# Optimization experiments

Hardware: AMD Instinct MI355X
Metric: run time of the kernel (lower is better)

Reference implementation:

```python
import jax, jax.numpy as jnp
import numpy as np

NUM_HEADS = 8
DIM_NODE, DIM_EDGE, DIM_TIME, DIM_OUT = 512, 172, 100, 512
U_NODE, U_EDGE, U_TIME, NUM_DST, E = 100000, 8192, 50000, 16384, 131072


def _linear_params(k, fan_in, fan_out):
    # torch.nn.Linear default init: U(-1/sqrt(fan_in), 1/sqrt(fan_in))
    kw, kb = jax.random.split(k)
    bound = 1.0 / np.sqrt(fan_in)
    w = jax.random.uniform(kw, (fan_in, fan_out), jnp.float32, -bound, bound)
    b = jax.random.uniform(kb, (fan_out,), jnp.float32, -bound, bound)
    return w, b


def setup_inputs() -> dict:
    key = jax.random.key(0)
    ks = jax.random.split(key, 16)
    inp = {}
    inp["idx"] = jax.random.randint(ks[0], (E,), 0, NUM_DST, jnp.int32)
    inp["nodeData"] = jax.random.normal(ks[1], (U_NODE, DIM_NODE), jnp.float32)
    inp["node_inverse"] = jax.random.randint(ks[2], (E,), 0, U_NODE, jnp.int32)
    inp["node_dst_inverse"] = jax.random.randint(ks[3], (NUM_DST,), 0, U_NODE, jnp.int32)
    inp["efeat_unique"] = jax.random.normal(ks[4], (U_EDGE, DIM_EDGE), jnp.float32)
    inp["efeat_inverse"] = jax.random.randint(ks[5], (E,), 0, U_EDGE, jnp.int32)
    inp["time_unique"] = jax.random.normal(ks[6], (U_TIME, DIM_TIME), jnp.float32)
    inp["time_inverse"] = jax.random.randint(ks[7], (E,), 0, U_TIME, jnp.int32)
    inp["time_dst_unique"] = jax.random.normal(ks[8], (1, DIM_TIME), jnp.float32)
    inp["time_dst_inverse"] = jnp.zeros((NUM_DST,), jnp.int32)
    inp["wq_node_w"], inp["wq_node_b"] = _linear_params(ks[9], DIM_NODE, DIM_OUT)
    inp["wq_time_w"], inp["wq_time_b"] = _linear_params(ks[10], DIM_TIME, DIM_OUT)
    inp["wkv_node_w"], inp["wkv_node_b"] = _linear_params(ks[11], DIM_NODE, 2 * DIM_OUT)
    inp["wkv_edge_w"], inp["wkv_edge_b"] = _linear_params(ks[12], DIM_EDGE, 2 * DIM_OUT)
    inp["wkv_time_w"], inp["wkv_time_b"] = _linear_params(ks[13], DIM_TIME, 2 * DIM_OUT)
    return inp


def reference(idx, nodeData, node_inverse, node_dst_inverse, efeat_unique,
              efeat_inverse, time_unique, time_inverse, time_dst_unique,
              time_dst_inverse, wq_node_w, wq_node_b, wq_time_w, wq_time_b,
              wkv_node_w, wkv_node_b, wkv_edge_w, wkv_edge_b, wkv_time_w,
              wkv_time_b):
    # project on UNIQUE rows, then scatter via inverse indices (dedup pattern)
    q_node = (nodeData @ wq_node_w + wq_node_b)[node_dst_inverse]      # [num_dst, D]
    q_time = (time_dst_unique @ wq_time_w + wq_time_b)[time_dst_inverse]
    Q = (q_node + q_time)[idx]                                          # [E, D]
    z_node = (nodeData @ wkv_node_w + wkv_node_b)[node_inverse]         # [E, 2D]
    z_edge = (efeat_unique @ wkv_edge_w + wkv_edge_b)[efeat_inverse]
    z_time = (time_unique @ wkv_time_w + wkv_time_b)[time_inverse]
    Z = z_node + z_edge + z_time
    D = wq_node_w.shape[1]
    K, V = Z[:, :D], Z[:, D:]
    n = Q.shape[0]
    Qh = Q.reshape(n, NUM_HEADS, -1)
    Kh = K.reshape(n, NUM_HEADS, -1)
    Vh = V.reshape(n, NUM_HEADS, -1)
    attn = jnp.sum(Qh * Kh, axis=2)                                      # [E, H]
    attn = jnp.where(attn >= 0, attn, 0.2 * attn)                        # LeakyReLU(0.2)
    return attn, Vh
```

## Files before the change

kernel.cpp:

```cpp
#include <hip/hip_runtime.h>
#include <hip/hip_bf16.h>

typedef __bf16 bf16_t;
typedef __bf16 bf16x8 __attribute__((ext_vector_type(8)));
typedef float  f32x4  __attribute__((ext_vector_type(4)));

#define E_NUM   131072
#define NDST    16384
#define DN      512
#define DE      172
#define DEP     192
#define DT      100
#define DTP     128
#define DO      512
#define KTOT    832
#define VBASE   (E_NUM * 8)

typedef const __attribute__((address_space(1))) char gbl_t;
typedef __attribute__((address_space(3))) char lds_t;

#define GLOAD_LDS16(g, l) __builtin_amdgcn_global_load_lds((gbl_t*)(g), (lds_t*)(l), 16, 0, 0)

__global__ void cvt_bf16_vec(const float* __restrict__ src, bf16_t* __restrict__ dst, long n8) {
    long i = (long)blockIdx.x * blockDim.x + threadIdx.x;
    long stride = (long)gridDim.x * blockDim.x;
    for (; i < n8; i += stride) {
        const float4* p = reinterpret_cast<const float4*>(src + i * 8);
        float4 a = p[0], b = p[1];
        union { bf16_t h[8]; uint4 q; } t;
        t.h[0]=(bf16_t)a.x; t.h[1]=(bf16_t)a.y; t.h[2]=(bf16_t)a.z; t.h[3]=(bf16_t)a.w;
        t.h[4]=(bf16_t)b.x; t.h[5]=(bf16_t)b.y; t.h[6]=(bf16_t)b.z; t.h[7]=(bf16_t)b.w;
        *reinterpret_cast<uint4*>(dst + i * 8) = t.q;
    }
}

__global__ void cvt_pad(const float* __restrict__ src, bf16_t* __restrict__ dst,
                        int rows, int cin, int cout) {
    long total = (long)rows * cout;
    long i = (long)blockIdx.x * blockDim.x + threadIdx.x;
    long stride = (long)gridDim.x * blockDim.x;
    for (; i < total; i += stride) {
        int r = (int)(i / cout), c = (int)(i - (long)r * cout);
        dst[i] = (c < cin) ? (bf16_t)src[(size_t)r * cin + c] : (bf16_t)0.0f;
    }
}

__global__ void prep_wkvT(const float* __restrict__ wn, const float* __restrict__ we,
                          const float* __restrict__ wt, const float* __restrict__ bn,
                          const float* __restrict__ be, const float* __restrict__ bt,
                          bf16_t* __restrict__ WkvT, float* __restrict__ kvbias) {
    int n = blockIdx.x;
    for (int k = threadIdx.x; k < KTOT; k += blockDim.x) {
        float v;
        if (k < 512)            v = wn[(size_t)k * 1024 + n];
        else if (k < 512 + DE)  v = we[(size_t)(k - 512) * 1024 + n];
        else if (k < 704)       v = 0.0f;
        else if (k < 704 + DT)  v = wt[(size_t)(k - 704) * 1024 + n];
        else                    v = 0.0f;
        WkvT[(size_t)n * KTOT + k] = (bf16_t)v;
    }
    if (threadIdx.x == 0) kvbias[n] = bn[n] + be[n] + bt[n];
}

__global__ void prep_wqT(const float* __restrict__ wq, bf16_t* __restrict__ WqT) {
    int n = blockIdx.x;
    for (int k = threadIdx.x; k < DO; k += blockDim.x)
        WqT[(size_t)n * DO + k] = (bf16_t)wq[(size_t)k * DO + n];
}

__global__ void prep_qbias(const float* __restrict__ td, const float* __restrict__ wqt,
                           const float* __restrict__ bqt, const float* __restrict__ bqn,
                           float* __restrict__ qbias) {
    int n = blockIdx.x * blockDim.x + threadIdx.x;
    if (n < DO) {
        float s = bqt[n] + bqn[n];
        for (int k = 0; k < DT; ++k) s += td[k] * wqt[(size_t)k * DO + n];
        qbias[n] = s;
    }
}

__global__ __launch_bounds__(256) void qd_gemm_kernel(
    const bf16_t* __restrict__ node_bf, const int* __restrict__ node_dst,
    const bf16_t* __restrict__ WqT, const float* __restrict__ qbias,
    float* __restrict__ QD) {
    const int bx = ((blockIdx.x & 7) << 6) + (blockIdx.x >> 3);
    const int mt = bx >> 2, nt = bx & 3;
    const int d0 = mt * 128, n0 = nt * 128;
    const int tid = threadIdx.x;
    const int lane = tid & 63, wid = tid >> 6;
    const int wm = wid >> 1, wn = wid & 1;
    const int lr = lane & 15, lg = lane >> 4;

    __shared__ __align__(16) bf16_t Ash[2][128 * 32];
    __shared__ __align__(16) bf16_t Bsh[2][128 * 32];

    const int srow = wid * 32 + (lane >> 2);
    const int csrc = ((lane & 3) - ((lane >> 3) & 3)) & 3;
    const bf16_t* pa0 = node_bf + (size_t)node_dst[d0 + srow] * DN + csrc * 8;
    const bf16_t* pa1 = node_bf + (size_t)node_dst[d0 + srow + 16] * DN + csrc * 8;
    const bf16_t* pb0 = WqT + (size_t)(n0 + srow) * DO + csrc * 8;
    const bf16_t* pb1 = pb0 + (size_t)16 * DO;

#define QD_STAGE(buf, kt) do {                                                   \
        int k0_ = (kt) * 32;                                                     \
        GLOAD_LDS16(pa0 + k0_, &Ash[buf][0] + wid * 1024);                       \
        GLOAD_LDS16(pa1 + k0_, &Ash[buf][0] + wid * 1024 + 512);                 \
        GLOAD_LDS16(pb0 + k0_, &Bsh[buf][0] + wid * 1024);                       \
        GLOAD_LDS16(pb1 + k0_, &Bsh[buf][0] + wid * 1024 + 512);                 \
    } while (0)

    f32x4 acc[4][4];
#pragma unroll
    for (int i = 0; i < 4; ++i)
#pragma unroll
        for (int j = 0; j < 4; ++j) { acc[i][j][0]=0.f; acc[i][j][1]=0.f; acc[i][j][2]=0.f; acc[i][j][3]=0.f; }

    const int rchk = ((lg + (lr >> 1)) & 3) * 8;

    QD_STAGE(0, 0);
    __syncthreads();
    int cur = 0;
    for (int kt = 0; kt < 16; ++kt) {
        if (kt < 15) QD_STAGE(cur ^ 1, kt + 1);
        bf16x8 af[4], bfr[4];
#pragma unroll
        for (int mi = 0; mi < 4; ++mi)
            af[mi] = *reinterpret_cast<const bf16x8*>(&Ash[cur][(wm * 64 + mi * 16 + lr) * 32 + rchk]);
#pragma unroll
        for (int ni = 0; ni < 4; ++ni)
            bfr[ni] = *reinterpret_cast<const bf16x8*>(&Bsh[cur][(wn * 64 + ni * 16 + lr) * 32 + rchk]);
#pragma unroll
        for (int mi = 0; mi < 4; ++mi)
#pragma unroll
            for (int ni = 0; ni < 4; ++ni)
                acc[mi][ni] = __builtin_amdgcn_mfma_f32_16x16x32_bf16(af[mi], bfr[ni], acc[mi][ni], 0, 0, 0);
        __syncthreads();
        cur ^= 1;
    }

    float qb[4];
#pragma unroll
    for (int ni = 0; ni < 4; ++ni) qb[ni] = qbias[n0 + wn * 64 + ni * 16 + lr];
#pragma unroll
    for (int mi = 0; mi < 4; ++mi)
#pragma unroll
        for (int j = 0; j < 4; ++j) {
            int m = wm * 64 + mi * 16 + lg * 4 + j;
            float* op = QD + (size_t)(d0 + m) * DO + n0 + wn * 64 + lr;
#pragma unroll
            for (int ni = 0; ni < 4; ++ni) op[ni * 16] = acc[mi][ni][j] + qb[ni];
        }
#undef QD_STAGE
}

__global__ __launch_bounds__(512) void kv_attn_kernel(
    const bf16_t* __restrict__ node_bf, const bf16_t* __restrict__ edge_bf,
    const bf16_t* __restrict__ time_bf, const int* __restrict__ node_inverse,
    const int* __restrict__ efeat_inverse, const int* __restrict__ time_inverse,
    const int* __restrict__ idx, const bf16_t* __restrict__ WkvT,
    const float* __restrict__ kvbias, const float* __restrict__ QD,
    float* __restrict__ out) {
    const int bx = ((blockIdx.x & 7) << 9) + (blockIdx.x >> 3);
    const int mt = bx >> 2, nt = bx & 3;
    const int e0 = mt * 128, n0 = nt * 256;
    const int tid = threadIdx.x;
    const int lane = tid & 63, wid = tid >> 6;
    const int wm = wid >> 2, wn = wid & 3;
    const int lr = lane & 15, lg = lane >> 4;

    __shared__ __align__(16) bf16_t Ash[2][128 * 32];
    __shared__ __align__(16) bf16_t Bsh[2][256 * 32];
    __shared__ int qrow_s[128];

    if (tid < 128) qrow_s[tid] = idx[e0 + tid];

    const int csrc = ((lane & 3) - ((lane >> 3) & 3)) & 3;
    const int arow = wid * 16 + (lane >> 2);
    const int ae = e0 + arow;
    const bf16_t* pn = node_bf + (size_t)node_inverse[ae] * DN  + csrc * 8;
    const bf16_t* pe = edge_bf + (size_t)efeat_inverse[ae] * DEP + csrc * 8;
    const bf16_t* pt = time_bf + (size_t)time_inverse[ae] * DTP + csrc * 8;
    const int brow = wid * 32 + (lane >> 2);
    const bf16_t* pb0 = WkvT + (size_t)(n0 + brow) * KTOT + csrc * 8;
    const bf16_t* pb1 = pb0 + (size_t)16 * KTOT;

#define KV_STAGE(buf, kt) do {                                                   \
        int k0_ = (kt) * 32;                                                     \
        const bf16_t* ga_;                                                       \
        if (k0_ < 512)      ga_ = pn + k0_;                                      \
        else if (k0_ < 704) ga_ = pe + (k0_ - 512);                              \
        else                ga_ = pt + (k0_ - 704);                              \
        GLOAD_LDS16(ga_,       &Ash[buf][0] + wid * 512);                        \
        GLOAD_LDS16(pb0 + k0_, &Bsh[buf][0] + wid * 1024);                       \
        GLOAD_LDS16(pb1 + k0_, &Bsh[buf][0] + wid * 1024 + 512);                 \
    } while (0)

    f32x4 acc[4][4];
#pragma unroll
    for (int i = 0; i < 4; ++i)
#pragma unroll
        for (int j = 0; j < 4; ++j) { acc[i][j][0]=0.f; acc[i][j][1]=0.f; acc[i][j][2]=0.f; acc[i][j][3]=0.f; }

    const int rchk = ((lg + (lr >> 1)) & 3) * 8;

    KV_STAGE(0, 0);
    __syncthreads();
    int cur = 0;
    for (int kt = 0; kt < 26; ++kt) {
        if (kt < 25) KV_STAGE(cur ^ 1, kt + 1);
        bf16x8 af[4], bfr[4];
#pragma unroll
        for (int mi = 0; mi < 4; ++mi)
            af[mi] = *reinterpret_cast<const bf16x8*>(&Ash[cur][(wm * 64 + mi * 16 + lr) * 32 + rchk]);
#pragma unroll
        for (int ni = 0; ni < 4; ++ni)
            bfr[ni] = *reinterpret_cast<const bf16x8*>(&Bsh[cur][(wn * 64 + ni * 16 + lr) * 32 + rchk]);
#pragma unroll
        for (int mi = 0; mi < 4; ++mi)
#pragma unroll
            for (int ni = 0; ni < 4; ++ni)
                acc[mi][ni] = __builtin_amdgcn_mfma_f32_16x16x32_bf16(af[mi], bfr[ni], acc[mi][ni], 0, 0, 0);
        __syncthreads();
        cur ^= 1;
    }
#undef KV_STAGE

    float kvb[4];
#pragma unroll
    for (int ni = 0; ni < 4; ++ni) kvb[ni] = kvbias[n0 + wn * 64 + ni * 16 + lr];

    if (nt < 2) {
        const int head = nt * 4 + wn;
        const int hcol = head * 64;
        float p[4][4];
#pragma unroll
        for (int mi = 0; mi < 4; ++mi)
#pragma unroll
            for (int j = 0; j < 4; ++j) {
                int m = wm * 64 + mi * 16 + lg * 4 + j;
                int qr = qrow_s[m];
                const float* qp = QD + (size_t)qr * DO + hcol + lr;
                float s = 0.f;
#pragma unroll
                for (int ni = 0; ni < 4; ++ni)
                    s += (acc[mi][ni][j] + kvb[ni]) * qp[ni * 16];
                p[mi][j] = s;
            }
#pragma unroll
        for (int off = 1; off < 16; off <<= 1)
#pragma unroll
            for (int mi = 0; mi < 4; ++mi)
#pragma unroll
                for (int j = 0; j < 4; ++j)
                    p[mi][j] += __shfl_xor(p[mi][j], off, 64);
        if (lr == 0) {
#pragma unroll
            for (int mi = 0; mi < 4; ++mi)
#pragma unroll
                for (int j = 0; j < 4; ++j) {
                    int e = e0 + wm * 64 + mi * 16 + lg * 4 + j;
                    float s = p[mi][j];
                    out[(size_t)e * 8 + head] = (s >= 0.f) ? s : 0.2f * s;
                }
        }
    } else {
        const int vcol0 = n0 - 512 + wn * 64;
#pragma unroll
        for (int mi = 0; mi < 4; ++mi)
#pragma unroll
            for (int j = 0; j < 4; ++j) {
                int e = e0 + wm * 64 + mi * 16 + lg * 4 + j;
                float* op = out + VBASE + (size_t)e * 512 + vcol0 + lr;
#pragma unroll
                for (int ni = 0; ni < 4; ++ni) op[ni * 16] = acc[mi][ni][j] + kvb[ni];
            }
    }
}

extern "C" void kernel_launch(void* const* d_in, const int* in_sizes, int n_in,
                              void* d_out, int out_size, void* d_ws, size_t ws_size,
                              hipStream_t stream) {
    const int*   idx        = (const int*)d_in[0];
    const float* nodeData   = (const float*)d_in[1];
    const int*   node_inv   = (const int*)d_in[2];
    const int*   node_dst   = (const int*)d_in[3];
    const float* efeat      = (const float*)d_in[4];
    const int*   efeat_inv  = (const int*)d_in[5];
    const float* time_u     = (const float*)d_in[6];
    const int*   time_inv   = (const int*)d_in[7];
    const float* time_dst   = (const float*)d_in[8];
    const float* wq_node_w  = (const float*)d_in[10];
    const float* wq_node_b  = (const float*)d_in[11];
    const float* wq_time_w  = (const float*)d_in[12];
    const float* wq_time_b  = (const float*)d_in[13];
    const float* wkv_node_w = (const float*)d_in[14];
    const float* wkv_node_b = (const float*)d_in[15];
    const float* wkv_edge_w = (const float*)d_in[16];
    const float* wkv_edge_b = (const float*)d_in[17];
    const float* wkv_time_w = (const float*)d_in[18];
    const float* wkv_time_b = (const float*)d_in[19];

    char* ws = (char*)d_ws;
    bf16_t* node_bf = (bf16_t*)(ws + 0);
    bf16_t* edge_bf = (bf16_t*)(ws + 102400000);
    bf16_t* time_bf = (bf16_t*)(ws + 105545728);
    bf16_t* WkvT    = (bf16_t*)(ws + 118345728);
    bf16_t* WqT     = (bf16_t*)(ws + 120049664);
    float*  kvbias  = (float*)(ws + 120573952);
    float*  qbias   = (float*)(ws + 120578048);
    float*  QD      = (float*)(ws + 120580096);
    float*  out     = (float*)d_out;

    cvt_bf16_vec<<<2048, 256, 0, stream>>>(nodeData, node_bf, (long)100000 * 512 / 8);
    cvt_pad<<<512, 256, 0, stream>>>(efeat, edge_bf, 8192, DE, DEP);
    cvt_pad<<<1024, 256, 0, stream>>>(time_u, time_bf, 50000, DT, DTP);
    prep_wkvT<<<1024, 256, 0, stream>>>(wkv_node_w, wkv_edge_w, wkv_time_w,
                                        wkv_node_b, wkv_edge_b, wkv_time_b, WkvT, kvbias);
    prep_wqT<<<512, 256, 0, stream>>>(wq_node_w, WqT);
    prep_qbias<<<2, 256, 0, stream>>>(time_dst, wq_time_w, wq_time_b, wq_node_b, qbias);
    qd_gemm_kernel<<<512, 256, 0, stream>>>(node_bf, node_dst, WqT, qbias, QD);
    kv_attn_kernel<<<4096, 512, 0, stream>>>(node_bf, edge_bf, time_bf, node_inv,
                                             efeat_inv, time_inv, idx, WkvT, kvbias, QD, out);
}
```

Measured before the change: 407.7 us.

## Software-pipeline gathered A rows through registers with explicit waitcnt scheduling

The gathered A-operand rows (node/edge/time features) now load into registers two k-steps ahead and are written to LDS after the MFMAs, while B still uses direct global-to-LDS loads. Explicit vmcnt/lgkmcnt waits, raw s_barrier, sched_barrier fences and s_setprio around the MFMA block replace __syncthreads and let the compiler-chosen order be fixed by hand. The aim is to hide the latency of the irregular gathers behind compute and to avoid the full waits __syncthreads inserts. The cost is more registers and a fragile hand-tuned wait count: vmcnt(1) must match the number of loads in flight.

```diff
diff --git a/kernel.cpp b/kernel.cpp
--- a/kernel.cpp
+++ b/kernel.cpp
@@ -20,6 +20,11 @@
 typedef __attribute__((address_space(3))) char lds_t;
 
 #define GLOAD_LDS16(g, l) __builtin_amdgcn_global_load_lds((gbl_t*)(g), (lds_t*)(l), 16, 0, 0)
+
+#define SCHEDB() __builtin_amdgcn_sched_barrier(0)
+#define WAITVM(n) do { asm volatile("s_waitcnt vmcnt(" #n ")" ::: "memory"); SCHEDB(); } while (0)
+#define LGKM0()   do { asm volatile("s_waitcnt lgkmcnt(0)" ::: "memory"); SCHEDB(); } while (0)
+#define RAWBAR()  do { SCHEDB(); __builtin_amdgcn_s_barrier(); SCHEDB(); } while (0)
 
 __global__ void cvt_bf16_vec(const float* __restrict__ src, bf16_t* __restrict__ dst, long n8) {
     long i = (long)blockIdx.x * blockDim.x + threadIdx.x;
@@ -177,22 +182,23 @@
     const int csrc = ((lane & 3) - ((lane >> 3) & 3)) & 3;
     const int arow = wid * 16 + (lane >> 2);
     const int ae = e0 + arow;
-    const bf16_t* pn = node_bf + (size_t)node_inverse[ae] * DN  + csrc * 8;
-    const bf16_t* pe = edge_bf + (size_t)efeat_inverse[ae] * DEP + csrc * 8;
-    const bf16_t* pt = time_bf + (size_t)time_inverse[ae] * DTP + csrc * 8;
+    const char* pnB = (const char*)(node_bf + (size_t)node_inverse[ae] * DN  + csrc * 8);
+    const char* peB = (const char*)(edge_bf + (size_t)efeat_inverse[ae] * DEP + csrc * 8);
+    const char* ptB = (const char*)(time_bf + (size_t)time_inverse[ae] * DTP + csrc * 8);
     const int brow = wid * 32 + (lane >> 2);
     const bf16_t* pb0 = WkvT + (size_t)(n0 + brow) * KTOT + csrc * 8;
     const bf16_t* pb1 = pb0 + (size_t)16 * KTOT;
 
-#define KV_STAGE(buf, kt) do {                                                   \
-        int k0_ = (kt) * 32;                                                     \
-        const bf16_t* ga_;                                                       \
-        if (k0_ < 512)      ga_ = pn + k0_;                                      \
-        else if (k0_ < 704) ga_ = pe + (k0_ - 512);                              \
-        else                ga_ = pt + (k0_ - 704);                              \
-        GLOAD_LDS16(ga_,       &Ash[buf][0] + wid * 512);                        \
-        GLOAD_LDS16(pb0 + k0_, &Bsh[buf][0] + wid * 1024);                       \
-        GLOAD_LDS16(pb1 + k0_, &Bsh[buf][0] + wid * 1024 + 512);                 \
+    bf16_t* const awrA0 = &Ash[0][wid * 512 + lane * 8];
+    bf16_t* const awrA1 = &Ash[1][wid * 512 + lane * 8];
+
+#define A_ADDR(ts_) ((ts_) < 16 ? pnB + (ts_) * 64                               \
+                     : (ts_) < 22 ? peB + ((ts_) - 16) * 64                      \
+                                  : ptB + ((ts_) - 22) * 64)
+#define B_ISSUE(buf_, tb_) do {                                                  \
+        int k0_ = (tb_) * 32;                                                    \
+        GLOAD_LDS16(pb0 + k0_, &Bsh[buf_][0] + wid * 1024);                      \
+        GLOAD_LDS16(pb1 + k0_, &Bsh[buf_][0] + wid * 1024 + 512);                 \
     } while (0)
 
     f32x4 acc[4][4];
@@ -203,27 +209,79 @@
 
     const int rchk = ((lg + (lr >> 1)) & 3) * 8;
 
-    KV_STAGE(0, 0);
-    __syncthreads();
-    int cur = 0;
-    for (int kt = 0; kt < 26; ++kt) {
-        if (kt < 25) KV_STAGE(cur ^ 1, kt + 1);
+#define DS_AB(p_, af_, bfr_) do {                                                 \
+        _Pragma("unroll")                                                         \
+        for (int mi = 0; mi < 4; ++mi)                                            \
+            af_[mi] = *reinterpret_cast<const bf16x8*>(&Ash[p_][(wm * 64 + mi * 16 + lr) * 32 + rchk]); \
+        _Pragma("unroll")                                                         \
+        for (int ni = 0; ni < 4; ++ni)                                            \
+            bfr_[ni] = *reinterpret_cast<const bf16x8*>(&Bsh[p_][(wn * 64 + ni * 16 + lr) * 32 + rchk]); \
+    } while (0)
+
+#define MFMAS(af_, bfr_) do {                                                     \
+        __builtin_amdgcn_s_setprio(1);                                            \
+        _Pragma("unroll")                                                         \
+        for (int mi = 0; mi < 4; ++mi)                                            \
+        _Pragma("unroll")                                                         \
+        for (int ni = 0; ni < 4; ++ni)                                            \
+            acc[mi][ni] = __builtin_amdgcn_mfma_f32_16x16x32_bf16(af_[mi], bfr_[ni], acc[mi][ni], 0, 0, 0); \
+        __builtin_amdgcn_s_setprio(0);                                            \
+    } while (0)
+
+#define STEP_FULL(kt_, p_, q_, awrq_, aCur_, aNext_) do {                         \
+        bf16x8 af[4], bfr[4];                                                     \
+        DS_AB(p_, af, bfr);                                                       \
+        SCHEDB();                                                                 \
+        B_ISSUE(q_, (kt_) + 1);                                                   \
+        SCHEDB();                                                                 \
+        aNext_ = *reinterpret_cast<const f32x4*>(A_ADDR((kt_) + 2));              \
+        SCHEDB();                                                                 \
+        MFMAS(af, bfr);                                                           \
+        SCHEDB();                                                                 \
+        *reinterpret_cast<f32x4*>(awrq_) = aCur_;        \
+        WAITVM(1);                                                                \
+        LGKM0();                                                                  \
+        RAWBAR();                                                                 \
+    } while (0)
+
+    f32x4 aP0, aP1;
+    aP0 = *reinterpret_cast<const f32x4*>(A_ADDR(0));
+    B_ISSUE(0, 0);
+    aP1 = *reinterpret_cast<const f32x4*>(A_ADDR(1));
+    SCHEDB();
+    *reinterpret_cast<f32x4*>(awrA0) = aP0;
+    WAITVM(1);
+    LGKM0();
+    RAWBAR();
+
+#pragma unroll
+    for (int kt = 0; kt < 24; kt += 2) {
+        STEP_FULL(kt,     0, 1, awrA1, aP1, aP0);
+        STEP_FULL(kt + 1, 1, 0, awrA0, aP0, aP1);
+    }
+    {
         bf16x8 af[4], bfr[4];
-#pragma unroll
-        for (int mi = 0; mi < 4; ++mi)
-            af[mi] = *reinterpret_cast<const bf16x8*>(&Ash[cur][(wm * 64 + mi * 16 + lr) * 32 + rchk]);
-#pragma unroll
-        for (int ni = 0; ni < 4; ++ni)
-            bfr[ni] = *reinterpret_cast<const bf16x8*>(&Bsh[cur][(wn * 64 + ni * 16 + lr) * 32 + rchk]);
-#pragma unroll
-        for (int mi = 0; mi < 4; ++mi)
-#pragma unroll
-            for (int ni = 0; ni < 4; ++ni)
-                acc[mi][ni] = __builtin_amdgcn_mfma_f32_16x16x32_bf16(af[mi], bfr[ni], acc[mi][ni], 0, 0, 0);
-        __syncthreads();
-        cur ^= 1;
-    }
-#undef KV_STAGE
+        DS_AB(0, af, bfr);
+        SCHEDB();
+        B_ISSUE(1, 25);
+        SCHEDB();
+        MFMAS(af, bfr);
+        SCHEDB();
+        *reinterpret_cast<f32x4*>(awrA1) = aP1;
+        WAITVM(0);
+        LGKM0();
+        RAWBAR();
+    }
+    {
+        bf16x8 af[4], bfr[4];
+        DS_AB(1, af, bfr);
+        MFMAS(af, bfr);
+    }
+#undef STEP_FULL
+#undef MFMAS
+#undef DS_AB
+#undef B_ISSUE
+#undef A_ADDR
 
     float kvb[4];
 #pragma unroll
```

Result: slower. 492.8 us (+20.9%).
